# Kernel optimization log

Hardware: AMD Instinct MI355X
Metric: run time of the kernel (lower is better)

Reference implementation:

```python
import jax, jax.numpy as jnp
import numpy as np

B, C, O, K, H, W, R = 32, 256, 256, 3, 56, 56, 16  # batch, in, out, kernel, spatial, reduction

def setup_inputs() -> dict:
    key = jax.random.key(0)
    ks = jax.random.split(key, 10)
    x = jax.random.normal(ks[0], (B, C, H, W), jnp.float32)
    # kaiming_normal fan_out: std = sqrt(2 / (O * K * K))
    base_w = jax.random.normal(ks[1], (O, C, K, K), jnp.float32) * np.sqrt(2.0 / (O * K * K))
    def lin(kw, kb, out_f, in_f):
        bound = 1.0 / np.sqrt(in_f)
        w = jax.random.uniform(kw, (out_f, in_f), jnp.float32, -bound, bound)
        b = jax.random.uniform(kb, (out_f,), jnp.float32, -bound, bound)
        return w, b
    fc_share_w, fc_share_b = lin(ks[2], ks[3], R, C)
    fc_inp_w, fc_inp_b = lin(ks[4], ks[5], C, R)   # in_planes // groups = C
    fc_oup_w, fc_oup_b = lin(ks[6], ks[7], O, R)
    fc_k_w, fc_k_b = lin(ks[8], ks[9], K * K, R)
    return {"x": x, "base_w": base_w,
            "fc_share_w": fc_share_w, "fc_share_b": fc_share_b,
            "fc_inp_w": fc_inp_w, "fc_inp_b": fc_inp_b,
            "fc_oup_w": fc_oup_w, "fc_oup_b": fc_oup_b,
            "fc_k_w": fc_k_w, "fc_k_b": fc_k_b}

def reference(x, base_w, fc_share_w, fc_share_b, fc_inp_w, fc_inp_b,
              fc_oup_w, fc_oup_b, fc_k_w, fc_k_b):
    # Attn4d: global avg pool -> shared FC -> three sigmoid branches
    s = jnp.mean(x, axis=(2, 3))                                   # [B, C]
    h = jax.nn.relu(s @ fc_share_w.T + fc_share_b)                 # [B, R]
    a_inp = jax.nn.sigmoid(h @ fc_inp_w.T + fc_inp_b)              # [B, C]
    a_oup = jax.nn.sigmoid(h @ fc_oup_w.T + fc_oup_b)              # [B, O]
    a_k = jax.nn.sigmoid(h @ fc_k_w.T + fc_k_b)                    # [B, K*K]
    # rank-1 outer products -> per-sample 4D attention [B, O, C, K, K]
    attn = jnp.einsum('bo,bi,bk->boik', a_oup, a_inp, a_k)
    attn = attn.reshape(x.shape[0], base_w.shape[0], base_w.shape[1],
                        base_w.shape[2], base_w.shape[3])
    w = base_w[None] * attn                                        # [B, O, C, K, K]
    # per-sample conv (equivalent to the groups=B grouped-conv trick)
    def conv1(xi, wi):
        return jax.lax.conv_general_dilated(
            xi[None], wi, window_strides=(1, 1),
            padding=((1, 1), (1, 1)),
            dimension_numbers=('NCHW', 'OIHW', 'NCHW'))[0]
    return jax.vmap(conv1)(x, w)                                   # [B, O, H, W]
```

## Files before the change

kernel.cpp:

```cpp
#include <hip/hip_runtime.h>


typedef __attribute__((ext_vector_type(8))) short s16x8;
typedef __attribute__((ext_vector_type(4))) float fx4;

#define PP_FIRST 59
#define XTP_ROWS 3456

__device__ __forceinline__ unsigned short bf16_rne(float f){
  unsigned u = __builtin_bit_cast(unsigned, f);
  u += 0x7fffu + ((u >> 16) & 1u);
  return (unsigned short)(u >> 16);
}
__device__ __forceinline__ float bf16_to_f(unsigned short h){
  unsigned u = ((unsigned)h) << 16;
  return __builtin_bit_cast(float, u);
}

__global__ void pool_kernel(const float* __restrict__ x, float* __restrict__ s){
  const int bc = blockIdx.x;
  const float* p = x + (size_t)bc * 3136;
  const int t = threadIdx.x;
  float sum = 0.f;
  for(int i = t; i < 784; i += 256){
    float4 v = ((const float4*)p)[i];
    sum += v.x + v.y + v.z + v.w;
  }
  for(int o = 32; o > 0; o >>= 1) sum += __shfl_down(sum, o);
  __shared__ float red[4];
  if((t & 63) == 0) red[t >> 6] = sum;
  __syncthreads();
  if(t == 0) s[bc] = (red[0] + red[1] + red[2] + red[3]) * (1.0f / 3136.0f);
}

__global__ void fc_kernel(const float* __restrict__ s,
                          const float* __restrict__ shw, const float* __restrict__ shb,
                          const float* __restrict__ inw, const float* __restrict__ inb,
                          const float* __restrict__ ouw, const float* __restrict__ oub,
                          const float* __restrict__ kw,  const float* __restrict__ kb,
                          float* __restrict__ a_inp, float* __restrict__ aoup_s,
                          float* __restrict__ rho, int* __restrict__ tpk){
  __shared__ float hh[32*16];
  __shared__ float ak[32*9];
  __shared__ float akmax[32];
  const int t = threadIdx.x;
  for(int i = t; i < 512; i += 256){
    int b = i >> 4, r = i & 15;
    float acc = shb[r];
    const float* sp = s + b*256; const float* wp = shw + r*256;
    for(int c = 0; c < 256; ++c) acc += sp[c] * wp[c];
    hh[i] = fmaxf(acc, 0.f);
  }
  __syncthreads();
  for(int i = t; i < 288; i += 256){
    int b = i / 9, k = i % 9;
    float acc = kb[k];
    for(int r = 0; r < 16; ++r) acc += hh[b*16+r] * kw[k*16+r];
    ak[i] = 1.f / (1.f + expf(-acc));
  }
  __syncthreads();
  if(t < 32){
    float v[9]; int id[9];
    for(int j = 0; j < 9; ++j){ v[j] = ak[t*9 + j]; id[j] = j; }
    for(int a = 1; a < 9; ++a){
      float vv = v[a]; int ii = id[a]; int p = a - 1;
      while(p >= 0 && v[p] > vv){ v[p+1] = v[p]; id[p+1] = id[p]; --p; }
      v[p+1] = vv; id[p+1] = ii;
    }
    for(int j = 0; j < 9; ++j){
      tpk[t*32 + 2*j]     = id[j];
      tpk[t*32 + 2*j + 1] = (id[j]/3 - 1)*58 + (id[j]%3 - 1);
    }
    for(int j = 0; j < 8; ++j) rho[t*8 + j] = v[j] / v[j+1];
    akmax[t] = v[8];
  }
  __syncthreads();
  for(int i = t; i < 8192; i += 256){
    int b = i >> 8, c = i & 255;
    float acc = inb[c];
    for(int r = 0; r < 16; ++r) acc += hh[b*16+r] * inw[c*16+r];
    a_inp[i] = 1.f / (1.f + expf(-acc));
  }
  for(int i = t; i < 8192; i += 256){
    int b = i >> 8, o = i & 255;
    float acc = oub[o];
    for(int r = 0; r < 16; ++r) acc += hh[b*16+r] * ouw[o*16+r];
    aoup_s[i] = (1.f / (1.f + expf(-acc))) * akmax[b];
  }
}

__global__ void wsplit_kernel(const float* __restrict__ bw,
                              unsigned short* __restrict__ wt_hi,
                              unsigned short* __restrict__ wt_lo){
  const int i = blockIdx.x * 256 + threadIdx.x;
  const float* p = bw + (size_t)i * 9;
  const int o = i >> 8, c = i & 255;
  #pragma unroll
  for(int k = 0; k < 9; ++k){
    float v = p[k];
    unsigned short h = bf16_rne(v);
    unsigned short l = bf16_rne(v - bf16_to_f(h));
    size_t idx = ((size_t)k << 16) + ((size_t)o << 8) + c;
    wt_hi[idx] = h; wt_lo[idx] = l;
  }
}

__global__ void zpad_kernel(unsigned short* __restrict__ xtp){
  const int slot = blockIdx.x, r = blockIdx.y;
  const int row = (r < 59) ? r : (3305 + (r - 59));
  xtp[((size_t)slot * XTP_ROWS + row) * 256 + threadIdx.x] = 0;
}

__global__ void xsplit_kernel(const float* __restrict__ x, const float* __restrict__ a_inp,
                              unsigned short* __restrict__ xtp, int b0){
  const int c0 = blockIdx.x * 64, h = blockIdx.y;
  const int slot = blockIdx.z, b = b0 + slot;
  __shared__ float tile[64 * 59];
  __shared__ float ainp_s[64];
  const int t = threadIdx.x;
  if(t < 64) ainp_s[t] = a_inp[(b << 8) + c0 + t];
  const float* xb = x + ((size_t)b * 256 + c0) * 3136 + h * 56;
  for(int i = t; i < 1792; i += 256){
    int c = i / 28, w2 = (i % 28) * 2;
    float2 v = *(const float2*)(xb + (size_t)c * 3136 + w2);
    tile[c * 59 + w2]     = v.x;
    tile[c * 59 + w2 + 1] = v.y;
  }
  __syncthreads();
  const size_t base = ((size_t)slot * XTP_ROWS + (size_t)(h + 1) * 58) * 256 + c0;
  for(int i = t; i < 58 * 32; i += 256){
    int wp = i >> 5, cp = (i & 31) * 2;
    float v0 = 0.f, v1 = 0.f;
    if(wp >= 1 && wp <= 56){
      v0 = tile[cp * 59 + (wp - 1)] * ainp_s[cp];
      v1 = tile[(cp + 1) * 59 + (wp - 1)] * ainp_s[cp + 1];
    }
    unsigned short h0 = bf16_rne(v0), h1 = bf16_rne(v1);
    *(unsigned*)(xtp + base + (size_t)wp * 256 + cp) = (unsigned)h0 | ((unsigned)h1 << 16);
  }
}

#define GLDS(gp, lo_) __builtin_amdgcn_global_load_lds( \
    (const __attribute__((address_space(1))) void*)(gp), \
    (__attribute__((address_space(3))) void*)(lds + (lo_)), 16, 0, 0)

__launch_bounds__(256, 2)
__global__ void conv_kernel(const unsigned short* __restrict__ wt_hi,
                            const unsigned short* __restrict__ wt_lo,
                            const unsigned short* __restrict__ xtp,
                            const float* __restrict__ aoup_s,
                            const float* __restrict__ rho,
                            const int* __restrict__ tpk,
                            float* __restrict__ out, int b0){
  __shared__ unsigned char lds[65536];
  const int tile = blockIdx.x;
  const int o0   = blockIdx.y << 7;
  const int slot = blockIdx.z;
  const int b    = b0 + slot;
  const int pp0  = PP_FIRST + tile * 256;
  const int t    = threadIdx.x;
  const int lane = t & 63;
  const int wave = t >> 6;
  const int wm = wave >> 1, wn = wave & 1;

  fx4 acc[4][8];
  #pragma unroll
  for(int i = 0; i < 4; ++i)
    #pragma unroll
    for(int j = 0; j < 8; ++j)
      acc[i][j] = fx4{0.f, 0.f, 0.f, 0.f};

  const int srow = t >> 3;
  const int sg8  = (((t & 7) ^ ((t >> 3) & 7)) << 3);
  const int ldsu = wave << 10;

  const int rA  = lane & 15;
  const int kg  = lane >> 4;
  const int r7  = rA & 7;
  const int gk0 = ((kg ^ r7) << 4);
  const int gk1 = (((4 + kg) ^ r7) << 4);
  const int aRow = ((wm << 6) + rA) * 128;
  const int bRow = ((wn << 7) + rA) * 128;

  const size_t xrow0 = (size_t)slot * XTP_ROWS * 256;

  for(int tap = 0; tap < 9; ++tap){
    if(tap > 0){
      const float rr = rho[(b << 3) + tap - 1];
      #pragma unroll
      for(int i = 0; i < 4; ++i)
        #pragma unroll
        for(int j = 0; j < 8; ++j)
          #pragma unroll
          for(int r = 0; r < 4; ++r) acc[i][j][r] *= rr;
    }
    const int pt  = tpk[(b << 5) + (tap << 1)];
    const int off = tpk[(b << 5) + (tap << 1) + 1];
    const unsigned short* xp  = xtp + xrow0 + (size_t)(pp0 + off + srow) * 256 + sg8;
    const unsigned short* wh0 = wt_hi + ((size_t)(pt * 256 + o0 + srow)) * 256 + sg8;
    const unsigned short* wl0 = wt_lo + ((size_t)(pt * 256 + o0 + srow)) * 256 + sg8;

    for(int cc = 0; cc < 4; ++cc){
      const int co = cc << 6;
      #pragma unroll
      for(int rnd = 0; rnd < 8; ++rnd)
        GLDS(xp + co + rnd * 8192, 0 + rnd * 4096 + ldsu);
      #pragma unroll
      for(int rnd = 0; rnd < 4; ++rnd){
        GLDS(wh0 + co + rnd * 8192, 32768 + rnd * 4096 + ldsu);
        GLDS(wl0 + co + rnd * 8192, 49152 + rnd * 4096 + ldsu);
      }
      __syncthreads();
      #pragma unroll
      for(int ks = 0; ks < 2; ++ks){
        const int gk = ks ? gk1 : gk0;
        s16x8 ah[4], al[4], bh[8];
        #pragma unroll
        for(int i = 0; i < 4; ++i){
          const int ro = aRow + i * 2048 + gk;
          ah[i] = *(const s16x8*)(lds + 32768 + ro);
          al[i] = *(const s16x8*)(lds + 49152 + ro);
        }
        #pragma unroll
        for(int j = 0; j < 8; ++j)
          bh[j] = *(const s16x8*)(lds + bRow + j * 2048 + gk);
        #pragma unroll
        for(int i = 0; i < 4; ++i)
          #pragma unroll
          for(int j = 0; j < 8; ++j){
            acc[i][j] = __builtin_amdgcn_mfma_f32_16x16x32_bf16(ah[i], bh[j], acc[i][j], 0, 0, 0);
            acc[i][j] = __builtin_amdgcn_mfma_f32_16x16x32_bf16(al[i], bh[j], acc[i][j], 0, 0, 0);
          }
      }
      __syncthreads();
    }
  }

  float sc[4][4];
  #pragma unroll
  for(int i = 0; i < 4; ++i){
    const int ob = o0 + (wm << 6) + i * 16 + (kg << 2);
    #pragma unroll
    for(int r = 0; r < 4; ++r) sc[i][r] = aoup_s[(b << 8) + ob + r];
  }
  #pragma unroll
  for(int j = 0; j < 8; ++j){
    const int pp = pp0 + (wn << 7) + j * 16 + rA;
    const int hp = pp / 58, wp = pp % 58;
    if(hp >= 1 && hp <= 56 && wp >= 1 && wp <= 56){
      const int p = (hp - 1) * 56 + (wp - 1);
      #pragma unroll
      for(int i = 0; i < 4; ++i){
        const int ob = o0 + (wm << 6) + i * 16 + (kg << 2);
        float* op = out + ((size_t)((b << 8) + ob)) * 3136 + p;
        #pragma unroll
        for(int r = 0; r < 4; ++r) op[(size_t)r * 3136] = acc[i][j][r] * sc[i][r];
      }
    }
  }
}

extern "C" void kernel_launch(void* const* d_in, const int* in_sizes, int n_in,
                              void* d_out, int out_size, void* d_ws, size_t ws_size,
                              hipStream_t stream){
  const float* x   = (const float*)d_in[0];
  const float* bw  = (const float*)d_in[1];
  const float* shw = (const float*)d_in[2];
  const float* shb = (const float*)d_in[3];
  const float* inw = (const float*)d_in[4];
  const float* inb = (const float*)d_in[5];
  const float* ouw = (const float*)d_in[6];
  const float* oub = (const float*)d_in[7];
  const float* kw  = (const float*)d_in[8];
  const float* kb  = (const float*)d_in[9];
  float* out = (float*)d_out;

  char* ws = (char*)d_ws;
  float* s      = (float*)(ws);
  float* a_inp  = (float*)(ws + 32768);
  float* aoup_s = (float*)(ws + 65536);
  float* rho    = (float*)(ws + 98304);
  int*   tpk    = (int*)(ws + 99328);
  unsigned short* wt_hi = (unsigned short*)(ws + 103424);
  unsigned short* wt_lo = wt_hi + 9 * 256 * 256;
  unsigned short* xtp   = (unsigned short*)(ws + 2462720);

  const size_t FIXED = 2462720;
  const size_t PERB  = (size_t)XTP_ROWS * 256 * 2;
  const size_t avail = ws_size > FIXED ? ws_size - FIXED : 0;
  size_t chs = avail / PERB; if(chs > 32) chs = 32; if(chs < 1) chs = 1;
  const int CH = (int)chs;

  hipLaunchKernelGGL(pool_kernel,   dim3(8192), dim3(256), 0, stream, x, s);
  hipLaunchKernelGGL(fc_kernel,     dim3(1),    dim3(256), 0, stream,
                     s, shw, shb, inw, inb, ouw, oub, kw, kb, a_inp, aoup_s, rho, tpk);
  hipLaunchKernelGGL(wsplit_kernel, dim3(256),  dim3(256), 0, stream, bw, wt_hi, wt_lo);
  hipLaunchKernelGGL(zpad_kernel,   dim3(CH, 210), dim3(256), 0, stream, xtp);
  for(int b0 = 0; b0 < 32; b0 += CH){
    const int z = (32 - b0 < CH) ? (32 - b0) : CH;
    hipLaunchKernelGGL(xsplit_kernel, dim3(4, 56, z), dim3(256), 0, stream, x, a_inp, xtp, b0);
    hipLaunchKernelGGL(conv_kernel,   dim3(13, 2, z), dim3(256), 0, stream,
                       wt_hi, wt_lo, xtp, aoup_s, rho, tpk, out, b0);
  }
}
```

Measured before the change: 484.9 us.

## Fuse pooling into input bf16 conversion and fold input attention into per-sample weights

```diff
diff --git a/kernel.cpp b/kernel.cpp
--- a/kernel.cpp
+++ b/kernel.cpp
@@ -17,20 +17,48 @@
   return __builtin_bit_cast(float, u);
 }
 
-__global__ void pool_kernel(const float* __restrict__ x, float* __restrict__ s){
-  const int bc = blockIdx.x;
-  const float* p = x + (size_t)bc * 3136;
+__global__ void zpad_kernel(unsigned short* __restrict__ xtp, float* __restrict__ s){
+  const int slot = blockIdx.x, r = blockIdx.y;
   const int t = threadIdx.x;
-  float sum = 0.f;
-  for(int i = t; i < 784; i += 256){
-    float4 v = ((const float4*)p)[i];
-    sum += v.x + v.y + v.z + v.w;
-  }
-  for(int o = 32; o > 0; o >>= 1) sum += __shfl_down(sum, o);
-  __shared__ float red[4];
-  if((t & 63) == 0) red[t >> 6] = sum;
+  if(r == 0) s[(slot << 8) + t] = 0.f;
+  const int row = (r < 59) ? r : (3305 + (r - 59));
+  xtp[((size_t)slot * XTP_ROWS + row) * 256 + t] = 0;
+}
+
+__global__ void xpool_kernel(const float* __restrict__ x,
+                             unsigned short* __restrict__ xtp,
+                             float* __restrict__ s){
+  const int c0 = blockIdx.x * 64, h = blockIdx.y;
+  const int b = blockIdx.z;
+  __shared__ float tile[64 * 59];
+  const int t = threadIdx.x;
+  const float* xb = x + ((size_t)b * 256 + c0) * 3136 + h * 56;
+  for(int i = t; i < 1792; i += 256){
+    int c = i / 28, w2 = (i % 28) * 2;
+    float2 v = *(const float2*)(xb + (size_t)c * 3136 + w2);
+    tile[c * 59 + w2]     = v.x;
+    tile[c * 59 + w2 + 1] = v.y;
+  }
   __syncthreads();
-  if(t == 0) s[bc] = (red[0] + red[1] + red[2] + red[3]) * (1.0f / 3136.0f);
+  {
+    const int c = t >> 2, q = t & 3;
+    float sm = 0.f;
+    for(int w = q; w < 56; w += 4) sm += tile[c * 59 + w];
+    sm += __shfl_down(sm, 2, 4);
+    sm += __shfl_down(sm, 1, 4);
+    if(q == 0) atomicAdd(&s[(b << 8) + c0 + c], sm);
+  }
+  const size_t base = ((size_t)b * XTP_ROWS + (size_t)(h + 1) * 58) * 256 + c0;
+  for(int i = t; i < 58 * 32; i += 256){
+    int wp = i >> 5, cp = (i & 31) * 2;
+    float v0 = 0.f, v1 = 0.f;
+    if(wp >= 1 && wp <= 56){
+      v0 = tile[cp * 59 + (wp - 1)];
+      v1 = tile[(cp + 1) * 59 + (wp - 1)];
+    }
+    unsigned short h0 = bf16_rne(v0), h1 = bf16_rne(v1);
+    *(unsigned*)(xtp + base + (size_t)wp * 256 + cp) = (unsigned)h0 | ((unsigned)h1 << 16);
+  }
 }
 
 __global__ void fc_kernel(const float* __restrict__ s,
@@ -46,10 +74,10 @@
   const int t = threadIdx.x;
   for(int i = t; i < 512; i += 256){
     int b = i >> 4, r = i & 15;
-    float acc = shb[r];
+    float dot = 0.f;
     const float* sp = s + b*256; const float* wp = shw + r*256;
-    for(int c = 0; c < 256; ++c) acc += sp[c] * wp[c];
-    hh[i] = fmaxf(acc, 0.f);
+    for(int c = 0; c < 256; ++c) dot += sp[c] * wp[c];
+    hh[i] = fmaxf(shb[r] + dot * (1.0f / 3136.0f), 0.f);
   }
   __syncthreads();
   for(int i = t; i < 288; i += 256){
@@ -89,54 +117,21 @@
   }
 }
 
-__global__ void wsplit_kernel(const float* __restrict__ bw,
+__global__ void wsplit_kernel(const float* __restrict__ bw, const float* __restrict__ a_inp,
                               unsigned short* __restrict__ wt_hi,
-                              unsigned short* __restrict__ wt_lo){
-  const int i = blockIdx.x * 256 + threadIdx.x;
-  const float* p = bw + (size_t)i * 9;
-  const int o = i >> 8, c = i & 255;
+                              unsigned short* __restrict__ wt_lo, int b0){
+  const int o = blockIdx.x, slot = blockIdx.y;
+  const int c = threadIdx.x;
+  const int b = b0 + slot;
+  const float ai = a_inp[(b << 8) + c];
+  const float* p = bw + ((size_t)o * 256 + c) * 9;
   #pragma unroll
   for(int k = 0; k < 9; ++k){
-    float v = p[k];
+    float v = p[k] * ai;
     unsigned short h = bf16_rne(v);
     unsigned short l = bf16_rne(v - bf16_to_f(h));
-    size_t idx = ((size_t)k << 16) + ((size_t)o << 8) + c;
+    size_t idx = (((size_t)slot * 9 + k) * 256 + o) * 256 + c;
     wt_hi[idx] = h; wt_lo[idx] = l;
-  }
-}
-
-__global__ void zpad_kernel(unsigned short* __restrict__ xtp){
-  const int slot = blockIdx.x, r = blockIdx.y;
-  const int row = (r < 59) ? r : (3305 + (r - 59));
-  xtp[((size_t)slot * XTP_ROWS + row) * 256 + threadIdx.x] = 0;
-}
-
-__global__ void xsplit_kernel(const float* __restrict__ x, const float* __restrict__ a_inp,
-                              unsigned short* __restrict__ xtp, int b0){
-  const int c0 = blockIdx.x * 64, h = blockIdx.y;
-  const int slot = blockIdx.z, b = b0 + slot;
-  __shared__ float tile[64 * 59];
-  __shared__ float ainp_s[64];
-  const int t = threadIdx.x;
-  if(t < 64) ainp_s[t] = a_inp[(b << 8) + c0 + t];
-  const float* xb = x + ((size_t)b * 256 + c0) * 3136 + h * 56;
-  for(int i = t; i < 1792; i += 256){
-    int c = i / 28, w2 = (i % 28) * 2;
-    float2 v = *(const float2*)(xb + (size_t)c * 3136 + w2);
-    tile[c * 59 + w2]     = v.x;
-    tile[c * 59 + w2 + 1] = v.y;
-  }
-  __syncthreads();
-  const size_t base = ((size_t)slot * XTP_ROWS + (size_t)(h + 1) * 58) * 256 + c0;
-  for(int i = t; i < 58 * 32; i += 256){
-    int wp = i >> 5, cp = (i & 31) * 2;
-    float v0 = 0.f, v1 = 0.f;
-    if(wp >= 1 && wp <= 56){
-      v0 = tile[cp * 59 + (wp - 1)] * ainp_s[cp];
-      v1 = tile[(cp + 1) * 59 + (wp - 1)] * ainp_s[cp + 1];
-    }
-    unsigned short h0 = bf16_rne(v0), h1 = bf16_rne(v1);
-    *(unsigned*)(xtp + base + (size_t)wp * 256 + cp) = (unsigned)h0 | ((unsigned)h1 << 16);
   }
 }
 
@@ -182,7 +177,8 @@
   const int aRow = ((wm << 6) + rA) * 128;
   const int bRow = ((wn << 7) + rA) * 128;
 
-  const size_t xrow0 = (size_t)slot * XTP_ROWS * 256;
+  const size_t xrow0 = (size_t)b * XTP_ROWS * 256;
+  const size_t wrow0 = (size_t)slot * 9 * 65536;
 
   for(int tap = 0; tap < 9; ++tap){
     if(tap > 0){
@@ -197,8 +193,8 @@
     const int pt  = tpk[(b << 5) + (tap << 1)];
     const int off = tpk[(b << 5) + (tap << 1) + 1];
     const unsigned short* xp  = xtp + xrow0 + (size_t)(pp0 + off + srow) * 256 + sg8;
-    const unsigned short* wh0 = wt_hi + ((size_t)(pt * 256 + o0 + srow)) * 256 + sg8;
-    const unsigned short* wl0 = wt_lo + ((size_t)(pt * 256 + o0 + srow)) * 256 + sg8;
+    const unsigned short* wh0 = wt_hi + wrow0 + ((size_t)(pt * 256 + o0 + srow)) * 256 + sg8;
+    const unsigned short* wl0 = wt_lo + wrow0 + ((size_t)(pt * 256 + o0 + srow)) * 256 + sg8;
 
     for(int cc = 0; cc < 4; ++cc){
       const int co = cc << 6;
@@ -281,24 +277,23 @@
   float* aoup_s = (float*)(ws + 65536);
   float* rho    = (float*)(ws + 98304);
   int*   tpk    = (int*)(ws + 99328);
-  unsigned short* wt_hi = (unsigned short*)(ws + 103424);
-  unsigned short* wt_lo = wt_hi + 9 * 256 * 256;
-  unsigned short* xtp   = (unsigned short*)(ws + 2462720);
-
-  const size_t FIXED = 2462720;
-  const size_t PERB  = (size_t)XTP_ROWS * 256 * 2;
-  const size_t avail = ws_size > FIXED ? ws_size - FIXED : 0;
-  size_t chs = avail / PERB; if(chs > 32) chs = 32; if(chs < 1) chs = 1;
-  const int CH = (int)chs;
-
-  hipLaunchKernelGGL(pool_kernel,   dim3(8192), dim3(256), 0, stream, x, s);
-  hipLaunchKernelGGL(fc_kernel,     dim3(1),    dim3(256), 0, stream,
+  unsigned short* xtp   = (unsigned short*)(ws + 103424);
+  unsigned short* wt_hi = (unsigned short*)(ws + 56726528);
+
+  const size_t WBYTES = 2359296;
+  size_t chw = (ws_size > 56726528) ? (ws_size - 56726528) / WBYTES : 1;
+  if(chw > 32) chw = 32; if(chw < 1) chw = 1;
+  const int CH_W = (int)chw;
+  unsigned short* wt_lo = wt_hi + (size_t)CH_W * 9 * 65536;
+
+  hipLaunchKernelGGL(zpad_kernel,  dim3(32, 210), dim3(256), 0, stream, xtp, s);
+  hipLaunchKernelGGL(xpool_kernel, dim3(4, 56, 32), dim3(256), 0, stream, x, xtp, s);
+  hipLaunchKernelGGL(fc_kernel,    dim3(1), dim3(256), 0, stream,
                      s, shw, shb, inw, inb, ouw, oub, kw, kb, a_inp, aoup_s, rho, tpk);
-  hipLaunchKernelGGL(wsplit_kernel, dim3(256),  dim3(256), 0, stream, bw, wt_hi, wt_lo);
-  hipLaunchKernelGGL(zpad_kernel,   dim3(CH, 210), dim3(256), 0, stream, xtp);
-  for(int b0 = 0; b0 < 32; b0 += CH){
-    const int z = (32 - b0 < CH) ? (32 - b0) : CH;
-    hipLaunchKernelGGL(xsplit_kernel, dim3(4, 56, z), dim3(256), 0, stream, x, a_inp, xtp, b0);
+  for(int b0 = 0; b0 < 32; b0 += CH_W){
+    const int z = (32 - b0 < CH_W) ? (32 - b0) : CH_W;
+    hipLaunchKernelGGL(wsplit_kernel, dim3(256, z), dim3(256), 0, stream,
+                       bw, a_inp, wt_hi, wt_lo, b0);
     hipLaunchKernelGGL(conv_kernel,   dim3(13, 2, z), dim3(256), 0, stream,
                        wt_hi, wt_lo, xtp, aoup_s, rho, tpk, out, b0);
   }
```

New measurement: 516.4 us. 6.5% more time.
